# Performance work log

Measured on AMD Instinct MI355X. Metric: run time of the kernel, lower is better.

## Reference

```python
import jax, jax.numpy as jnp
import numpy as np

TEMPERATURE = 8.0  # sqrt(head_dim=64)
_MASKING_VALUE = -1e30  # float32 branch of the original module


def setup_inputs() -> dict:
    key = jax.random.key(0)
    kq, kk, kv = jax.random.split(key, 3)
    B, H, S, D = 2, 12, 2048, 64
    q = jax.random.normal(kq, (B, H, S, D), dtype=jnp.float32)
    k = jax.random.normal(kk, (B, H, S, D), dtype=jnp.float32)
    v = jax.random.normal(kv, (B, H, S, D), dtype=jnp.float32)
    # causal mask, broadcastable over batch and heads; mask==0 -> masked
    mask = jnp.tril(jnp.ones((S, S), dtype=jnp.bool_))[None, None, :, :]
    return {"q": q, "k": k, "v": v, "mask": mask}


def reference(q, k, v, mask):
    # attn = (q / temperature) @ k^T  -> [B,H,S,S]
    scores = jnp.einsum("bhqd,bhkd->bhqk", q / TEMPERATURE, k)
    scores = jnp.where(mask, scores, _MASKING_VALUE)
    attn = jax.nn.softmax(scores, axis=-1)  # dropout in eval mode (identity)
    output = jnp.einsum("bhqk,bhkd->bhqd", attn, v)
    return (output, attn)
```

## Files before the change

kernel.cpp:

```cpp
#include <hip/hip_runtime.h>
#include <hip/hip_bf16.h>
#include <stdint.h>

#define SS 2048
#define DD 64
#define NHEAD 24
#define TK 64
#define NKT 32

typedef __attribute__((ext_vector_type(8))) short short8;
typedef __attribute__((ext_vector_type(4))) short short4v;
typedef __attribute__((ext_vector_type(4))) float f32x4;

#define QSCALE 0.18033688011112042f
#define MLOG   46.166241308446828f

#if __has_builtin(__builtin_amdgcn_exp2f)
#define EXP2(x) __builtin_amdgcn_exp2f(x)
#else
#define EXP2(x) exp2f(x)
#endif

#if __has_builtin(__builtin_amdgcn_logf)
#define LOG2F(x) __builtin_amdgcn_logf(x)
#else
#define LOG2F(x) log2f(x)
#endif

__device__ __forceinline__ unsigned short f2bf(float x) {
  union { float f; unsigned u; } a; a.f = x;
  unsigned r = a.u + 0x7FFFu + ((a.u >> 16) & 1u);
  return (unsigned short)(r >> 16);
}
__device__ __forceinline__ float bf2f(unsigned short u) {
  union { unsigned u; float f; } a; a.u = ((unsigned)u) << 16;
  return a.f;
}

__device__ __forceinline__ void stage16(const unsigned char* g, unsigned char* l) {
  __builtin_amdgcn_global_load_lds(
      (const __attribute__((address_space(1))) unsigned int*)g,
      (__attribute__((address_space(3))) unsigned int*)l, 16, 0, 0);
}

__global__ __launch_bounds__(256) void prep_kernel(
    const float* __restrict__ q, const float* __restrict__ k,
    const float* __restrict__ v, unsigned short* __restrict__ qb,
    unsigned char* __restrict__ kb, unsigned char* __restrict__ vtb) {
  const int head = blockIdx.x >> 5;
  const int t64 = blockIdx.x & 31;
  const int tid = threadIdx.x;
  const int c4 = tid & 15;
  const size_t inbase = ((size_t)head * SS + (size_t)t64 * 64) * DD;
  const f32x4* qsrc = (const f32x4*)(q + inbase);
  const f32x4* ksrc = (const f32x4*)(k + inbase);
  const f32x4* vsrc = (const f32x4*)(v + inbase);
  unsigned short* qdst = qb + inbase;
  unsigned char* ktile = kb + ((size_t)(head * NKT + t64) << 13);
  unsigned char* vtile = vtb + ((size_t)(head * NKT + t64) << 13);
#pragma unroll
  for (int j = 0; j < 4; ++j) {
    const int row = (tid >> 4) + 16 * j;
    f32x4 xq = qsrc[row * 16 + c4];
    short4v hq;
    hq.x = (short)f2bf(xq.x * QSCALE); hq.y = (short)f2bf(xq.y * QSCALE);
    hq.z = (short)f2bf(xq.z * QSCALE); hq.w = (short)f2bf(xq.w * QSCALE);
    *(short4v*)(qdst + row * 64 + c4 * 4) = hq;

    f32x4 xk = ksrc[row * 16 + c4];
    short4v hk;
    hk.x = (short)f2bf(xk.x); hk.y = (short)f2bf(xk.y);
    hk.z = (short)f2bf(xk.z); hk.w = (short)f2bf(xk.w);
    const int chunk = c4 >> 1, half = c4 & 1;
    *(short4v*)(ktile + row * 128 + ((chunk ^ (row & 7)) << 4) + half * 8) = hk;

    f32x4 xv = vsrc[row * 16 + c4];
    float vals[4] = {xv.x, xv.y, xv.z, xv.w};
#pragma unroll
    for (int e = 0; e < 4; ++e) {
      const int d = c4 * 4 + e;
      *(unsigned short*)(vtile + d * 128 + (((row >> 3) ^ (d & 7)) << 4) +
                         (row & 7) * 2) = f2bf(vals[e]);
    }
  }
}

__global__ __launch_bounds__(256) void sdpa_kernel(
    const unsigned short* __restrict__ qb, const unsigned char* __restrict__ kb,
    const unsigned char* __restrict__ vtb, float* __restrict__ out,
    float* __restrict__ attn) {
  __shared__ unsigned char lds[40960];

  const int bid = blockIdx.x;
  const int xcd = bid & 7;
  const int seq = bid >> 3;
  const int head = xcd * 3 + (seq >> 5);
  const int qt = 31 - (seq & 31);
  const int q0 = qt * TK;

  const int tid = threadIdx.x;
  const int w = tid >> 6;
  const int l = tid & 63;
  const int lhi = l >> 4;
  const int llo = l & 15;
  const int qrl = 16 * w + llo;

  const unsigned short* qh = qb + (size_t)head * SS * DD;
  const unsigned char* kh = kb + ((size_t)(head * NKT) << 13);
  const unsigned char* vh = vtb + ((size_t)(head * NKT) << 13);
  float* oh = out + (size_t)head * SS * DD;
  float* ah = attn + (size_t)head * SS * SS;
  unsigned char* ldsP = lds + 32768;

  short8 qf0 = *(const short8*)(qh + (size_t)(q0 + qrl) * DD + lhi * 8);
  short8 qf1 = *(const short8*)(qh + (size_t)(q0 + qrl) * DD + lhi * 8 + 32);

  float lsum = 0.f;
  stage16(kh + tid * 16, lds + tid * 16);
  stage16(kh + 4096 + tid * 16, lds + 4096 + tid * 16);
  __syncthreads();
  int b = 0;
  for (int kt = 0; kt <= qt; ++kt) {
    if (kt < qt) {
      const unsigned char* src = kh + ((size_t)(kt + 1) << 13);
      unsigned char* dst = lds + (b ^ 1) * 8192;
      stage16(src + tid * 16, dst + tid * 16);
      stage16(src + 4096 + tid * 16, dst + 4096 + tid * 16);
    }
    const unsigned char* kbuf = lds + b * 8192;
    const bool diag = (kt == qt);
#pragma unroll
    for (int c = 0; c < 4; ++c) {
      const int br = 16 * c + llo;
      short8 kf0 = *(const short8*)(kbuf + br * 128 + ((lhi ^ (br & 7)) << 4));
      short8 kf1 = *(const short8*)(kbuf + br * 128 + (((lhi + 4) ^ (br & 7)) << 4));
      f32x4 acc = {0.f, 0.f, 0.f, 0.f};
      acc = __builtin_amdgcn_mfma_f32_16x16x32_bf16(kf0, qf0, acc, 0, 0, 0);
      acc = __builtin_amdgcn_mfma_f32_16x16x32_bf16(kf1, qf1, acc, 0, 0, 0);
#pragma unroll
      for (int r = 0; r < 4; ++r) {
        float sv = acc[r];
        if (diag && (16 * c + 4 * lhi + r > qrl)) sv = -INFINITY;
        lsum += EXP2(sv - MLOG);
      }
    }
    __syncthreads();
    b ^= 1;
  }
  lsum += __shfl_xor(lsum, 16);
  lsum += __shfl_xor(lsum, 32);
  const float ladj = MLOG + LOG2F(lsum);

  f32x4 o[4];
#pragma unroll
  for (int c = 0; c < 4; ++c) o[c] = (f32x4){0.f, 0.f, 0.f, 0.f};

  b = 0;
  stage16(kh + tid * 16, lds + tid * 16);
  stage16(kh + 4096 + tid * 16, lds + 4096 + tid * 16);
  stage16(vh + tid * 16, lds + 16384 + tid * 16);
  stage16(vh + 4096 + tid * 16, lds + 16384 + 4096 + tid * 16);
  __syncthreads();

  for (int kt = 0; kt <= qt; ++kt) {
    if (kt < qt) {
      const unsigned char* ksrc = kh + ((size_t)(kt + 1) << 13);
      const unsigned char* vsrc = vh + ((size_t)(kt + 1) << 13);
      unsigned char* kdst = lds + (b ^ 1) * 8192;
      unsigned char* vdst = lds + 16384 + (b ^ 1) * 8192;
      stage16(ksrc + tid * 16, kdst + tid * 16);
      stage16(ksrc + 4096 + tid * 16, kdst + 4096 + tid * 16);
      stage16(vsrc + tid * 16, vdst + tid * 16);
      stage16(vsrc + 4096 + tid * 16, vdst + 4096 + tid * 16);
    }
    const unsigned char* kbuf = lds + b * 8192;
    const unsigned char* vbuf = lds + 16384 + b * 8192;
    const bool diag = (kt == qt);

#pragma unroll
    for (int c = 0; c < 4; ++c) {
      const int br = 16 * c + llo;
      short8 kf0 = *(const short8*)(kbuf + br * 128 + ((lhi ^ (br & 7)) << 4));
      short8 kf1 = *(const short8*)(kbuf + br * 128 + (((lhi + 4) ^ (br & 7)) << 4));
      f32x4 acc = {0.f, 0.f, 0.f, 0.f};
      acc = __builtin_amdgcn_mfma_f32_16x16x32_bf16(kf0, qf0, acc, 0, 0, 0);
      acc = __builtin_amdgcn_mfma_f32_16x16x32_bf16(kf1, qf1, acc, 0, 0, 0);
      float p[4];
#pragma unroll
      for (int r = 0; r < 4; ++r) {
        float s = acc[r];
        if (diag && (16 * c + 4 * lhi + r > qrl)) s = -INFINITY;
        p[r] = EXP2(s - ladj);
      }
      short4v hv;
      hv.x = (short)f2bf(p[0]); hv.y = (short)f2bf(p[1]);
      hv.z = (short)f2bf(p[2]); hv.w = (short)f2bf(p[3]);
      const int cc = 2 * c + (lhi >> 1);
      *(short4v*)(ldsP + qrl * 128 + ((cc ^ (qrl & 7)) << 4) + ((lhi & 1) << 3)) = hv;
    }

    asm volatile("s_waitcnt lgkmcnt(0)" ::: "memory");
    __builtin_amdgcn_s_barrier();
    __builtin_amdgcn_sched_barrier(0);

    {
      const int k0 = kt * TK;
      const int ro_b = (tid >> 4);
      const int cg = tid & 15;
#pragma unroll
      for (int j = 0; j < 4; ++j) {
        const int row = ro_b + 16 * j;
        short4v pv = *(const short4v*)(ldsP + row * 128 +
                                       (((cg >> 1) ^ (row & 7)) << 4) + ((cg & 1) << 3));
        f32x4 fo;
        fo.x = bf2f((unsigned short)pv.x);
        fo.y = bf2f((unsigned short)pv.y);
        fo.z = bf2f((unsigned short)pv.z);
        fo.w = bf2f((unsigned short)pv.w);
        *(f32x4*)(ah + (size_t)(q0 + row) * SS + k0 + cg * 4) = fo;
      }
    }

    {
      const int pr = 16 * w + llo;
      short8 pa0 = *(const short8*)(ldsP + pr * 128 + ((lhi ^ (pr & 7)) << 4));
      short8 pa1 = *(const short8*)(ldsP + pr * 128 + (((4 + lhi) ^ (pr & 7)) << 4));
#pragma unroll
      for (int c = 0; c < 4; ++c) {
        const int vr = 16 * c + llo;
        short8 vb0 = *(const short8*)(vbuf + vr * 128 + ((lhi ^ (vr & 7)) << 4));
        short8 vb1 = *(const short8*)(vbuf + vr * 128 + (((lhi + 4) ^ (vr & 7)) << 4));
        o[c] = __builtin_amdgcn_mfma_f32_16x16x32_bf16(pa0, vb0, o[c], 0, 0, 0);
        o[c] = __builtin_amdgcn_mfma_f32_16x16x32_bf16(pa1, vb1, o[c], 0, 0, 0);
      }
    }
    __syncthreads();
    b ^= 1;
  }

  {
    const int zc = (qt + 1) * TK;
    f32x4 z = {0.f, 0.f, 0.f, 0.f};
#pragma unroll
    for (int j = 0; j < 4; ++j) {
      int row = q0 + 16 * w + 4 * j + lhi;
      f32x4* dst = (f32x4*)(ah + (size_t)row * SS);
      for (int c = (zc >> 2) + llo; c < (SS >> 2); c += 16) dst[c] = z;
    }
  }

#pragma unroll
  for (int c = 0; c < 4; ++c)
#pragma unroll
    for (int r = 0; r < 4; ++r) {
      int qrow = q0 + 16 * w + 4 * lhi + r;
      oh[(size_t)qrow * DD + 16 * c + llo] = o[c][r];
    }
}

extern "C" void kernel_launch(void* const* d_in, const int* in_sizes, int n_in,
                              void* d_out, int out_size, void* d_ws, size_t ws_size,
                              hipStream_t stream) {
  const float* q = (const float*)d_in[0];
  const float* k = (const float*)d_in[1];
  const float* v = (const float*)d_in[2];
  float* out = (float*)d_out;
  float* attn = out + (size_t)NHEAD * SS * DD;

  const size_t QKV_BYTES = (size_t)NHEAD * SS * DD * 2;
  unsigned short* qb = (unsigned short*)d_ws;
  unsigned char* kb = (unsigned char*)d_ws + QKV_BYTES;
  unsigned char* vtb = kb + QKV_BYTES;

  prep_kernel<<<dim3(NHEAD * NKT), dim3(256), 0, stream>>>(q, k, v, qb, kb, vtb);
  sdpa_kernel<<<dim3(NHEAD * NKT), dim3(256), 0, stream>>>(qb, kb, vtb, out, attn);
}
```

Baseline: 476.5 us.

## Pipeline K staging deeper and use one barrier per attention tile

The first pass (row-sum) now uses a 4-slot K ring with prefetch distance two, synchronised by explicit vmcnt waits plus a single s_barrier per iteration instead of two __syncthreads. The second pass likewise moves to one wait-and-barrier at the top of each tile. Each wave now writes attn rows only from its own P rows, which removes the cross-wave barrier before the write-out. The aim is to cut barrier stalls and expose more load latency overlap, at the risk of subtle LDS races if the vmcnt counts or ring indexing are wrong.

```diff
diff --git a/kernel.cpp b/kernel.cpp
--- a/kernel.cpp
+++ b/kernel.cpp
@@ -118,16 +118,24 @@
   float lsum = 0.f;
   stage16(kh + tid * 16, lds + tid * 16);
   stage16(kh + 4096 + tid * 16, lds + 4096 + tid * 16);
-  __syncthreads();
-  int b = 0;
+  if (qt >= 1) {
+    stage16(kh + 8192 + tid * 16, lds + 8192 + tid * 16);
+    stage16(kh + 8192 + 4096 + tid * 16, lds + 8192 + 4096 + tid * 16);
+  }
   for (int kt = 0; kt <= qt; ++kt) {
     if (kt < qt) {
-      const unsigned char* src = kh + ((size_t)(kt + 1) << 13);
-      unsigned char* dst = lds + (b ^ 1) * 8192;
+      asm volatile("s_waitcnt vmcnt(2)\n\ts_barrier" ::: "memory");
+    } else {
+      asm volatile("s_waitcnt vmcnt(0)\n\ts_barrier" ::: "memory");
+    }
+    __builtin_amdgcn_sched_barrier(0);
+    if (kt + 2 <= qt) {
+      const unsigned char* src = kh + ((size_t)(kt + 2) << 13);
+      unsigned char* dst = lds + ((kt + 2) & 3) * 8192;
       stage16(src + tid * 16, dst + tid * 16);
       stage16(src + 4096 + tid * 16, dst + 4096 + tid * 16);
     }
-    const unsigned char* kbuf = lds + b * 8192;
+    const unsigned char* kbuf = lds + (kt & 3) * 8192;
     const bool diag = (kt == qt);
 #pragma unroll
     for (int c = 0; c < 4; ++c) {
@@ -144,37 +152,41 @@
         lsum += EXP2(sv - MLOG);
       }
     }
-    __syncthreads();
-    b ^= 1;
   }
   lsum += __shfl_xor(lsum, 16);
   lsum += __shfl_xor(lsum, 32);
   const float ladj = MLOG + LOG2F(lsum);
 
+  __syncthreads();
+
   f32x4 o[4];
 #pragma unroll
   for (int c = 0; c < 4; ++c) o[c] = (f32x4){0.f, 0.f, 0.f, 0.f};
 
-  b = 0;
   stage16(kh + tid * 16, lds + tid * 16);
   stage16(kh + 4096 + tid * 16, lds + 4096 + tid * 16);
   stage16(vh + tid * 16, lds + 16384 + tid * 16);
   stage16(vh + 4096 + tid * 16, lds + 16384 + 4096 + tid * 16);
-  __syncthreads();
 
   for (int kt = 0; kt <= qt; ++kt) {
+    if (kt == 0) {
+      asm volatile("s_waitcnt vmcnt(0)\n\ts_barrier" ::: "memory");
+    } else {
+      asm volatile("s_waitcnt vmcnt(4)\n\ts_barrier" ::: "memory");
+    }
+    __builtin_amdgcn_sched_barrier(0);
     if (kt < qt) {
       const unsigned char* ksrc = kh + ((size_t)(kt + 1) << 13);
       const unsigned char* vsrc = vh + ((size_t)(kt + 1) << 13);
-      unsigned char* kdst = lds + (b ^ 1) * 8192;
-      unsigned char* vdst = lds + 16384 + (b ^ 1) * 8192;
+      unsigned char* kdst = lds + ((kt + 1) & 1) * 8192;
+      unsigned char* vdst = lds + 16384 + ((kt + 1) & 1) * 8192;
       stage16(ksrc + tid * 16, kdst + tid * 16);
       stage16(ksrc + 4096 + tid * 16, kdst + 4096 + tid * 16);
       stage16(vsrc + tid * 16, vdst + tid * 16);
       stage16(vsrc + 4096 + tid * 16, vdst + 4096 + tid * 16);
     }
-    const unsigned char* kbuf = lds + b * 8192;
-    const unsigned char* vbuf = lds + 16384 + b * 8192;
+    const unsigned char* kbuf = lds + (kt & 1) * 8192;
+    const unsigned char* vbuf = lds + 16384 + (kt & 1) * 8192;
     const bool diag = (kt == qt);
 
 #pragma unroll
@@ -200,24 +212,24 @@
     }
 
     asm volatile("s_waitcnt lgkmcnt(0)" ::: "memory");
-    __builtin_amdgcn_s_barrier();
     __builtin_amdgcn_sched_barrier(0);
 
     {
       const int k0 = kt * TK;
-      const int ro_b = (tid >> 4);
-      const int cg = tid & 15;
+      const int row = 16 * w + (l >> 2);
+      float* arow = ah + (size_t)(q0 + row) * SS + k0;
+      const unsigned char* prow = ldsP + row * 128;
+      const int rs = row & 7;
 #pragma unroll
       for (int j = 0; j < 4; ++j) {
-        const int row = ro_b + 16 * j;
-        short4v pv = *(const short4v*)(ldsP + row * 128 +
-                                       (((cg >> 1) ^ (row & 7)) << 4) + ((cg & 1) << 3));
+        const int sc = (l & 3) + 4 * j;
+        short4v pv = *(const short4v*)(prow + (((sc >> 1) ^ rs) << 4) + ((sc & 1) << 3));
         f32x4 fo;
         fo.x = bf2f((unsigned short)pv.x);
         fo.y = bf2f((unsigned short)pv.y);
         fo.z = bf2f((unsigned short)pv.z);
         fo.w = bf2f((unsigned short)pv.w);
-        *(f32x4*)(ah + (size_t)(q0 + row) * SS + k0 + cg * 4) = fo;
+        *(f32x4*)(arow + sc * 4) = fo;
       }
     }
 
@@ -234,8 +246,6 @@
         o[c] = __builtin_amdgcn_mfma_f32_16x16x32_bf16(pa1, vb1, o[c], 0, 0, 0);
       }
     }
-    __syncthreads();
-    b ^= 1;
   }
 
   {
```

Result: no change. 480.8 us (+0.9%).
